# Performance work log

Measured on AMD Instinct MI355X. Metric: run time of the kernel, lower is better.

Reference implementation:

```python
import jax, jax.numpy as jnp
import numpy as np

N, T, K, R, DK = 4096, 8, 4, 8, 64
S = 2   # slot_dim (2D coords)
B = 20  # noise samples (hardcoded in original forward)


def _conv1d(x, w, b, pad):
    # x: [batch, Cin, L], w: [Cout, Cin, ks] (torch Conv1d layout == OIH)
    y = jax.lax.conv_general_dilated(x, w, (1,), [(pad, pad)],
                                     dimension_numbers=('NCH', 'OIH', 'NCH'))
    return y + b[None, :, None]


def setup_inputs() -> dict:
    key = jax.random.key(0)
    ks = iter(jax.random.split(key, 40))
    r = lambda shape, s=0.1: jax.random.normal(next(ks), shape, jnp.float32) * s
    return dict(
        obs=r((1, S, N, T), 1.0),
        obs_vel=r((1, S, N, T), 1.0),
        noise=r((B, 2, 1, 1), 1.0),
        wq_rule=r((S * T, DK)), bq_rule=r((DK,)),
        wq_ctx=r((2 * S * T, DK)), bq_ctx=r((DK,)),
        wk_ctx=r((2 * S * T, DK)), bk_ctx=r((DK,)),
        rule_emb=r((R, DK), 1.0),
        w_noise=r((R,), 1.0), w_indiv=r((R,), 1.0), w_social=r((R,), 1.0),
        sp_w=r((R, S, S * (K + 1), 3)), sp_b=r((R, S)),
        spr_w=r((R, S, S * (K + 1), 1)), spr_b=r((R, S)),
        tp_w=r((R, 12, T, 3)), tp_b=r((R, 12)),
        tpr_w=r((R, 12, T, 1)), tpr_b=r((R, 12)),
        spi_w=r((R, S, S, 3)), spi_b=r((R, S)),
        spir_w=r((R, S, S, 1)), spir_b=r((R, S)),
        tpi_w=r((R, 12, T, 3)), tpi_b=r((R, 12)),
        tpir_w=r((R, 12, T, 1)), tpir_b=r((R, 12)),
    )


def reference(obs, obs_vel, noise, wq_rule, bq_rule, wq_ctx, bq_ctx, wk_ctx, bk_ctx,
              rule_emb, w_noise, w_indiv, w_social,
              sp_w, sp_b, spr_w, spr_b, tp_w, tp_b, tpr_w, tpr_b,
              spi_w, spi_b, spir_w, spir_b, tpi_w, tpi_b, tpir_w, tpir_b):
    # ---- context selection (eval path: topk_onehot) ----
    cat = jnp.concatenate([obs, obs_vel], axis=1)[0]           # [2S, N, T]
    x_ctx = jnp.transpose(cat, (1, 2, 0)).reshape(N, -1)       # [N, T*2S]
    q = x_ctx @ wq_ctx + bq_ctx
    k_ = x_ctx @ wk_ctx + bk_ctx
    attn_ctx = jax.nn.softmax(q @ k_.T, axis=-1)               # [N, N]
    _, ctx_idx = jax.lax.top_k(attn_ctx, K)                    # [N, K]
    # gather == bmm with one-hot [N,N] masks in the original
    ov_node = jnp.transpose(obs_vel[0], (1, 0, 2))             # [N, S, T]
    ctx_vel = ov_node[ctx_idx]                                 # [N, K, S, T]
    ctx_vel = jnp.transpose(ctx_vel, (1, 2, 0, 3)).reshape(1, K * S, N, T)

    # ---- rule selection (hard top-1) ----
    x_rule = jnp.transpose(obs_vel[0], (1, 2, 0)).reshape(N, -1)  # [N, T*S]
    rq = x_rule @ wq_rule + bq_rule
    attn_rule = jax.nn.softmax(rq @ rule_emb.T, axis=-1)       # [N, R]
    rule_mask = jax.nn.one_hot(jnp.argmax(attn_rule, -1), R, dtype=obs.dtype)  # [N, R]

    noise_rep = jnp.tile(noise, (1, K, 1, 1))                  # [B, K*S, 1, 1]

    def rule_fn(wn, wi, ws, p):
        ov = obs_vel + noise * wn                              # [B, S, N, T]
        ov_f = jnp.transpose(ov, (0, 2, 1, 3)).reshape(B * N, S, T)
        cv = ctx_vel + noise_rep * wn                          # [B, K*S, N, T]
        cv_f = jnp.transpose(cv, (0, 2, 1, 3)).reshape(B * N, K * S, T)
        comb = jnp.concatenate([ov_f, cv_f], axis=1)           # [B*N, S*(K+1), T]
        si = jax.nn.relu(_conv1d(ov_f, p['spi_w'], p['spi_b'], 1)) \
             + _conv1d(ov_f, p['spir_w'], p['spir_b'], 0)      # [B*N, S, T]
        ti = jnp.transpose(si, (0, 2, 1))                      # [B*N, T, S]
        indiv = _conv1d(ti, p['tpi_w'], p['tpi_b'], 1) + _conv1d(ti, p['tpir_w'], p['tpir_b'], 0)
        ss = jax.nn.relu(_conv1d(comb, p['sp_w'], p['sp_b'], 1)) \
             + _conv1d(comb, p['spr_w'], p['spr_b'], 0)        # [B*N, S, T]
        ts = jnp.transpose(ss, (0, 2, 1))
        social = _conv1d(ts, p['tp_w'], p['tp_b'], 1) + _conv1d(ts, p['tpr_w'], p['tpr_b'], 0)
        return wi * indiv + ws * social                        # [B*N, 12, S]

    params = dict(sp_w=sp_w, sp_b=sp_b, spr_w=spr_w, spr_b=spr_b,
                  tp_w=tp_w, tp_b=tp_b, tpr_w=tpr_w, tpr_b=tpr_b,
                  spi_w=spi_w, spi_b=spi_b, spir_w=spir_w, spir_b=spir_b,
                  tpi_w=tpi_w, tpi_b=tpi_b, tpir_w=tpir_w, tpir_b=tpir_b)
    preds = jax.vmap(rule_fn)(w_noise, w_indiv, w_social, params)  # [R, B*N, 12, S]
    preds = preds.reshape(R, B, N, 12, S)
    # hard rule dispatch + final permute(0,2,3,1) of the original -> [B, N, 12, S]
    return jnp.einsum('rbnts,nr->bnts', preds, rule_mask)
```

## Files before the change

### kernel.cpp

```cpp
#include <hip/hip_runtime.h>
#include <cstdint>
#include <cstddef>

#define N_   4096
#define T_   8
#define K_   4
#define R_   8
#define DK_  64
#define S_   2
#define B_   20
#define NT_  (N_*T_)

__device__ __forceinline__ unsigned long long mkkey(float v, int col) {
    unsigned u = __float_as_uint(v);
    u = (u & 0x80000000u) ? ~u : (u | 0x80000000u);
    return ((unsigned long long)u << 32) | (unsigned)(~col);
}

#define INS4(t0,t1,t2,t3,keyexpr) do {                                  \
    unsigned long long _k = (keyexpr);                                  \
    if (_k > (t3)) {                                                    \
        bool _g2 = _k > (t2), _g1 = _k > (t1), _g0 = _k > (t0);         \
        (t3) = _g2 ? (t2) : _k;                                         \
        (t2) = _g2 ? (_g1 ? (t1) : _k) : (t2);                          \
        (t1) = _g1 ? (_g0 ? (t0) : _k) : (t1);                          \
        (t0) = _g0 ? _k : (t0);                                         \
    }                                                                   \
} while (0)

__global__ __launch_bounds__(64) void proj_kernel(
    const float* __restrict__ obs, const float* __restrict__ obsv,
    const float* __restrict__ wq_ctx, const float* __restrict__ bq_ctx,
    const float* __restrict__ wk_ctx, const float* __restrict__ bk_ctx,
    const float* __restrict__ wq_rule, const float* __restrict__ bq_rule,
    const float* __restrict__ rule_emb,
    float* __restrict__ qg, float* __restrict__ kg, int* __restrict__ rid)
{
    int n = blockIdx.x;
    int d = threadIdx.x;
    __shared__ float x[32];
    if (d < 32) {
        int t = d >> 2, c = d & 3;
        const float* src = (c < 2) ? obs : obsv;
        x[d] = src[(c & 1) * NT_ + n * T_ + t];
    }
    __syncthreads();
    float q = bq_ctx[d], k = bk_ctx[d], rq = bq_rule[d];
    #pragma unroll
    for (int i = 0; i < 32; ++i) {
        float xv = x[i];
        q = fmaf(xv, wq_ctx[i*64 + d], q);
        k = fmaf(xv, wk_ctx[i*64 + d], k);
    }
    #pragma unroll
    for (int i = 0; i < 16; ++i) {
        int t = i >> 1, s = i & 1;
        rq = fmaf(x[t*4 + 2 + s], wq_rule[i*64 + d], rq);
    }
    qg[n*64 + d] = q;
    kg[n*64 + d] = k;

    float best = -1e30f; int bestr = 0;
    #pragma unroll
    for (int r = 0; r < 8; ++r) {
        float p = rq * rule_emb[r*64 + d];
        #pragma unroll
        for (int off = 32; off > 0; off >>= 1) p += __shfl_xor(p, off, 64);
        if (p > best) { best = p; bestr = r; }
    }
    if (d == 0) rid[n] = bestr;
}

#define BM      16
#define CT      128
#define NSPLIT  4
#define KST     68
#define TILES   ((N_/NSPLIT)/CT)

__global__ __launch_bounds__(256) void attn_topk_kernel(
    const float* __restrict__ qg, const float* __restrict__ kg,
    unsigned long long* __restrict__ part)
{
    __shared__ union U {
        float ks[CT*KST];
        unsigned long long sc[BM*64*4];
    } u;
    __shared__ float qs[BM*64];

    int tid  = threadIdx.x;
    int lane = tid & 63, wv = tid >> 6;
    int rowblk = blockIdx.x / NSPLIT, split = blockIdx.x % NSPLIT;
    int row0 = rowblk * BM;
    int col0 = split * (N_ / NSPLIT);
    int r0 = wv * 4;

    ((float4*)qs)[tid] = ((const float4*)(qg + (size_t)row0*64))[tid];

    unsigned long long T0a=0,T0b=0,T0c=0,T0d=0;
    unsigned long long T1a=0,T1b=0,T1c=0,T1d=0;
    unsigned long long T2a=0,T2b=0,T2c=0,T2d=0;
    unsigned long long T3a=0,T3b=0,T3c=0,T3d=0;

    for (int tile = 0; tile < TILES; ++tile) {
        int c0 = col0 + tile * CT;
        __syncthreads();
        #pragma unroll
        for (int i = 0; i < 8; ++i) {
            int chunk = tid + 256*i;
            int c = chunk >> 4, dseg = chunk & 15;
            float4 v = *(const float4*)(kg + (size_t)(c0 + c)*64 + dseg*4);
            *(float4*)(&u.ks[c*KST + dseg*4]) = v;
        }
        __syncthreads();

        float a00=0.f,a01=0.f, a10=0.f,a11=0.f, a20=0.f,a21=0.f, a30=0.f,a31=0.f;

        #pragma unroll 4
        for (int d = 0; d < 64; d += 4) {
            float4 k0 = *(const float4*)(&u.ks[lane*KST + d]);
            float4 k1 = *(const float4*)(&u.ks[(lane+64)*KST + d]);
            float4 q0 = *(const float4*)(&qs[(r0+0)*64 + d]);
            float4 q1 = *(const float4*)(&qs[(r0+1)*64 + d]);
            float4 q2 = *(const float4*)(&qs[(r0+2)*64 + d]);
            float4 q3 = *(const float4*)(&qs[(r0+3)*64 + d]);
            a00 = fmaf(q0.w,k0.w, fmaf(q0.z,k0.z, fmaf(q0.y,k0.y, fmaf(q0.x,k0.x, a00))));
            a01 = fmaf(q0.w,k1.w, fmaf(q0.z,k1.z, fmaf(q0.y,k1.y, fmaf(q0.x,k1.x, a01))));
            a10 = fmaf(q1.w,k0.w, fmaf(q1.z,k0.z, fmaf(q1.y,k0.y, fmaf(q1.x,k0.x, a10))));
            a11 = fmaf(q1.w,k1.w, fmaf(q1.z,k1.z, fmaf(q1.y,k1.y, fmaf(q1.x,k1.x, a11))));
            a20 = fmaf(q2.w,k0.w, fmaf(q2.z,k0.z, fmaf(q2.y,k0.y, fmaf(q2.x,k0.x, a20))));
            a21 = fmaf(q2.w,k1.w, fmaf(q2.z,k1.z, fmaf(q2.y,k1.y, fmaf(q2.x,k1.x, a21))));
            a30 = fmaf(q3.w,k0.w, fmaf(q3.z,k0.z, fmaf(q3.y,k0.y, fmaf(q3.x,k0.x, a30))));
            a31 = fmaf(q3.w,k1.w, fmaf(q3.z,k1.z, fmaf(q3.y,k1.y, fmaf(q3.x,k1.x, a31))));
        }
        int cA = c0 + lane, cB = c0 + lane + 64;
        INS4(T0a,T0b,T0c,T0d, mkkey(a00, cA));
        INS4(T0a,T0b,T0c,T0d, mkkey(a01, cB));
        INS4(T1a,T1b,T1c,T1d, mkkey(a10, cA));
        INS4(T1a,T1b,T1c,T1d, mkkey(a11, cB));
        INS4(T2a,T2b,T2c,T2d, mkkey(a20, cA));
        INS4(T2a,T2b,T2c,T2d, mkkey(a21, cB));
        INS4(T3a,T3b,T3c,T3d, mkkey(a30, cA));
        INS4(T3a,T3b,T3c,T3d, mkkey(a31, cB));
    }

    __syncthreads();
    {
        unsigned long long* p = &u.sc[((size_t)(r0+0)*64 + lane)*4];
        p[0]=T0a; p[1]=T0b; p[2]=T0c; p[3]=T0d;
        p = &u.sc[((size_t)(r0+1)*64 + lane)*4];
        p[0]=T1a; p[1]=T1b; p[2]=T1c; p[3]=T1d;
        p = &u.sc[((size_t)(r0+2)*64 + lane)*4];
        p[0]=T2a; p[1]=T2b; p[2]=T2c; p[3]=T2d;
        p = &u.sc[((size_t)(r0+3)*64 + lane)*4];
        p[0]=T3a; p[1]=T3b; p[2]=T3c; p[3]=T3d;
    }
    __syncthreads();

    if (tid < BM) {
        unsigned long long m0=0,m1=0,m2=0,m3=0;
        const unsigned long long* p = &u.sc[(size_t)tid*64*4];
        for (int j = 0; j < 256; ++j) INS4(m0,m1,m2,m3, p[j]);
        int n = row0 + tid;
        unsigned long long* q = &part[(size_t)(n*NSPLIT + split)*4];
        q[0]=m0; q[1]=m1; q[2]=m2; q[3]=m3;
    }
}

__global__ __launch_bounds__(256) void merge_kernel(
    const unsigned long long* __restrict__ part, int* __restrict__ cidx)
{
    int n = blockIdx.x * blockDim.x + threadIdx.x;
    if (n >= N_) return;
    unsigned long long m0=0,m1=0,m2=0,m3=0;
    #pragma unroll
    for (int j = 0; j < NSPLIT*4; ++j) INS4(m0,m1,m2,m3, part[(size_t)n*NSPLIT*4 + j]);
    cidx[n*4 + 0] = (int)(~((unsigned)(m0 & 0xffffffffull)));
    cidx[n*4 + 1] = (int)(~((unsigned)(m1 & 0xffffffffull)));
    cidx[n*4 + 2] = (int)(~((unsigned)(m2 & 0xffffffffull)));
    cidx[n*4 + 3] = (int)(~((unsigned)(m3 & 0xffffffffull)));
}

#define WST 708

__global__ __launch_bounds__(256) void predict_kernel(
    const float* __restrict__ obsv, const float* __restrict__ noise,
    const float* __restrict__ w_noise, const float* __restrict__ w_indiv,
    const float* __restrict__ w_social,
    const float* __restrict__ sp_w, const float* __restrict__ sp_b,
    const float* __restrict__ spr_w, const float* __restrict__ spr_b,
    const float* __restrict__ tp_w, const float* __restrict__ tp_b,
    const float* __restrict__ tpr_w, const float* __restrict__ tpr_b,
    const float* __restrict__ spi_w, const float* __restrict__ spi_b,
    const float* __restrict__ spir_w, const float* __restrict__ spir_b,
    const float* __restrict__ tpi_w, const float* __restrict__ tpi_b,
    const float* __restrict__ tpir_w, const float* __restrict__ tpir_b,
    const int* __restrict__ rid, const int* __restrict__ cidx,
    float* __restrict__ out)
{
    __shared__ float W[R_*WST];
    __shared__ float nz_s[B_*2];
    __shared__ float wn_s[R_], wi_s[R_], ws_s[R_];
    int tid = threadIdx.x;

    for (int idx = tid; idx < R_*704; idx += 256) {
        int r = idx / 704, o = idx % 704;
        float v;
        if (o < 12)      v = spi_w[r*12 + o];
        else if (o < 16) v = spir_w[r*4 + (o-12)];
        else if (o < 76) v = sp_w[r*60 + (o-16)];
        else if (o < 96) v = spr_w[r*20 + (o-76)];
        else if (o < 192) { int q=o-96;  int t=q/12, co=q%12; v = tpi_w[((r*12+co)*8+t)*3+1] + tpir_w[(r*12+co)*8+t]; }
        else if (o < 288) { int q=o-192; int t=q/12, co=q%12; v = tpi_w[((r*12+co)*8+t)*3+2]; }
        else if (o < 384) { int q=o-288; int t=q/12, co=q%12; v = tpi_w[((r*12+co)*8+t)*3+0]; }
        else if (o < 480) { int q=o-384; int t=q/12, co=q%12; v = tp_w[((r*12+co)*8+t)*3+1] + tpr_w[(r*12+co)*8+t]; }
        else if (o < 576) { int q=o-480; int t=q/12, co=q%12; v = tp_w[((r*12+co)*8+t)*3+2]; }
        else if (o < 672) { int q=o-576; int t=q/12, co=q%12; v = tp_w[((r*12+co)*8+t)*3+0]; }
        else if (o < 674) v = spi_b[r*2 + (o-672)];
        else if (o < 676) v = spir_b[r*2 + (o-674)];
        else if (o < 678) v = sp_b[r*2 + (o-676)];
        else if (o < 680) v = spr_b[r*2 + (o-678)];
        else if (o < 692) v = tpi_b[r*12 + (o-680)] + tpir_b[r*12 + (o-680)];
        else              v = tp_b[r*12 + (o-692)] + tpr_b[r*12 + (o-692)];
        W[r*WST + o] = v;
    }
    if (tid < B_*2)                  nz_s[tid] = noise[tid];
    if (tid >= 64  && tid < 64+R_)   wn_s[tid-64]  = w_noise[tid-64];
    if (tid >= 96  && tid < 96+R_)   wi_s[tid-96]  = w_indiv[tid-96];
    if (tid >= 128 && tid < 128+R_)  ws_s[tid-128] = w_social[tid-128];
    __syncthreads();

    int item = blockIdx.x*256 + tid;
    if (item >= B_*N_) return;
    int n = item / B_, b = item - n*B_;
    int r = rid[n];
    const float* Wr = &W[r*WST];
    float wn = wn_s[r];
    float nz0 = nz_s[b*2+0]*wn, nz1 = nz_s[b*2+1]*wn;

    float x[10][8];
    #pragma unroll
    for (int s = 0; s < 2; ++s) {
        float4 a = *(const float4*)(obsv + s*NT_ + n*8);
        float4 c = *(const float4*)(obsv + s*NT_ + n*8 + 4);
        float nz = s ? nz1 : nz0;
        x[s][0]=a.x+nz; x[s][1]=a.y+nz; x[s][2]=a.z+nz; x[s][3]=a.w+nz;
        x[s][4]=c.x+nz; x[s][5]=c.y+nz; x[s][6]=c.z+nz; x[s][7]=c.w+nz;
    }
    #pragma unroll
    for (int k = 0; k < 4; ++k) {
        int cn = cidx[n*4 + k];
        #pragma unroll
        for (int s = 0; s < 2; ++s) {
            float4 a = *(const float4*)(obsv + s*NT_ + cn*8);
            float4 c = *(const float4*)(obsv + s*NT_ + cn*8 + 4);
            float nz = s ? nz1 : nz0;
            int ch = 2 + k*2 + s;
            x[ch][0]=a.x+nz; x[ch][1]=a.y+nz; x[ch][2]=a.z+nz; x[ch][3]=a.w+nz;
            x[ch][4]=c.x+nz; x[ch][5]=c.y+nz; x[ch][6]=c.z+nz; x[ch][7]=c.w+nz;
        }
    }

    float si[2][8];
    #pragma unroll
    for (int so = 0; so < 2; ++so) {
        float pre[8];
        float bb = Wr[672+so];
        #pragma unroll
        for (int t = 0; t < 8; ++t) pre[t] = bb;
        #pragma unroll
        for (int ci = 0; ci < 2; ++ci) {
            float w0 = Wr[so*6+ci*3+0], w1 = Wr[so*6+ci*3+1], w2 = Wr[so*6+ci*3+2];
            pre[0] += x[ci][0]*w1 + x[ci][1]*w2;
            #pragma unroll
            for (int t = 1; t < 7; ++t) pre[t] += x[ci][t-1]*w0 + x[ci][t]*w1 + x[ci][t+1]*w2;
            pre[7] += x[ci][6]*w0 + x[ci][7]*w1;
        }
        float l0 = Wr[12+so*2+0], l1 = Wr[12+so*2+1];
        float lb = Wr[674+so];
        #pragma unroll
        for (int t = 0; t < 8; ++t)
            si[so][t] = fmaxf(pre[t], 0.f) + lb + x[0][t]*l0 + x[1][t]*l1;
    }

    float ss[2][8];
    #pragma unroll
    for (int so = 0; so < 2; ++so) {
        float pre[8], lin[8];
        float bb = Wr[676+so], lb = Wr[678+so];
        #pragma unroll
        for (int t = 0; t < 8; ++t) { pre[t] = bb; lin[t] = lb; }
        #pragma unroll
        for (int ci = 0; ci < 10; ++ci) {
            float w0 = Wr[16+so*30+ci*3+0], w1 = Wr[16+so*30+ci*3+1], w2 = Wr[16+so*30+ci*3+2];
            float lw = Wr[76+so*10+ci];
            pre[0] += x[ci][0]*w1 + x[ci][1]*w2;
            #pragma unroll
            for (int t = 1; t < 7; ++t) pre[t] += x[ci][t-1]*w0 + x[ci][t]*w1 + x[ci][t+1]*w2;
            pre[7] += x[ci][6]*w0 + x[ci][7]*w1;
            #pragma unroll
            for (int t = 0; t < 8; ++t) lin[t] += x[ci][t]*lw;
        }
        #pragma unroll
        for (int t = 0; t < 8; ++t) ss[so][t] = fmaxf(pre[t], 0.f) + lin[t];
    }

    float i0[12], i1[12], s0a[12], s1a[12];
    #pragma unroll
    for (int co = 0; co < 12; ++co) {
        float bi = Wr[680+co], bs = Wr[692+co];
        i0[co]=bi; i1[co]=bi; s0a[co]=bs; s1a[co]=bs;
    }
    #pragma unroll
    for (int t = 0; t < 8; ++t) {
        float a0 = si[0][t], a1 = si[1][t];
        float b0 = ss[0][t], b1 = ss[1][t];
        #pragma unroll
        for (int co = 0; co < 12; ++co) {
            i0[co]  += a0*Wr[96 +t*12+co] + a1*Wr[192+t*12+co];
            i1[co]  += a1*Wr[96 +t*12+co] + a0*Wr[288+t*12+co];
            s0a[co] += b0*Wr[384+t*12+co] + b1*Wr[480+t*12+co];
            s1a[co] += b1*Wr[384+t*12+co] + b0*Wr[576+t*12+co];
        }
    }

    float wi = wi_s[r], wsoc = ws_s[r];
    float o[24];
    #pragma unroll
    for (int co = 0; co < 12; ++co) {
        o[co*2+0] = wi*i0[co] + wsoc*s0a[co];
        o[co*2+1] = wi*i1[co] + wsoc*s1a[co];
    }
    float* dst = out + (size_t)(b*N_ + n)*24;
    #pragma unroll
    for (int q4 = 0; q4 < 6; ++q4)
        *(float4*)(dst + q4*4) = *(const float4*)(&o[q4*4]);
}

extern "C" void kernel_launch(void* const* d_in, const int* in_sizes, int n_in,
                              void* d_out, int out_size, void* d_ws, size_t ws_size,
                              hipStream_t stream)
{
    const float* obs      = (const float*)d_in[0];
    const float* obsv     = (const float*)d_in[1];
    const float* noise    = (const float*)d_in[2];
    const float* wq_rule  = (const float*)d_in[3];
    const float* bq_rule  = (const float*)d_in[4];
    const float* wq_ctx   = (const float*)d_in[5];
    const float* bq_ctx   = (const float*)d_in[6];
    const float* wk_ctx   = (const float*)d_in[7];
    const float* bk_ctx   = (const float*)d_in[8];
    const float* rule_emb = (const float*)d_in[9];
    const float* w_noise  = (const float*)d_in[10];
    const float* w_indiv  = (const float*)d_in[11];
    const float* w_social = (const float*)d_in[12];
    const float* sp_w  = (const float*)d_in[13];
    const float* sp_b  = (const float*)d_in[14];
    const float* spr_w = (const float*)d_in[15];
    const float* spr_b = (const float*)d_in[16];
    const float* tp_w  = (const float*)d_in[17];
    const float* tp_b  = (const float*)d_in[18];
    const float* tpr_w = (const float*)d_in[19];
    const float* tpr_b = (const float*)d_in[20];
    const float* spi_w  = (const float*)d_in[21];
    const float* spi_b  = (const float*)d_in[22];
    const float* spir_w = (const float*)d_in[23];
    const float* spir_b = (const float*)d_in[24];
    const float* tpi_w  = (const float*)d_in[25];
    const float* tpi_b  = (const float*)d_in[26];
    const float* tpir_w = (const float*)d_in[27];
    const float* tpir_b = (const float*)d_in[28];

    char* ws = (char*)d_ws;
    float* qg = (float*)(ws);
    float* kg = (float*)(ws + 1048576);
    unsigned long long* part = (unsigned long long*)(ws + 2097152);
    int* rid  = (int*)(ws + 2621440);
    int* cidx = (int*)(ws + 2637824);

    hipLaunchKernelGGL(proj_kernel, dim3(N_), dim3(64), 0, stream,
        obs, obsv, wq_ctx, bq_ctx, wk_ctx, bk_ctx, wq_rule, bq_rule, rule_emb,
        qg, kg, rid);

    hipLaunchKernelGGL(attn_topk_kernel, dim3((N_/BM)*NSPLIT), dim3(256), 0, stream,
        qg, kg, part);

    hipLaunchKernelGGL(merge_kernel, dim3(N_/256), dim3(256), 0, stream,
        part, cidx);

    hipLaunchKernelGGL(predict_kernel, dim3((B_*N_)/256), dim3(256), 0, stream,
        obsv, noise, w_noise, w_indiv, w_social,
        sp_w, sp_b, spr_w, spr_b, tp_w, tp_b, tpr_w, tpr_b,
        spi_w, spi_b, spir_w, spir_b, tpi_w, tpi_b, tpir_w, tpir_b,
        rid, cidx, (float*)d_out);
}
```

Before: 238.5 us.

## Use 4x4 register-blocked outer-product tiling for attention top-k scoring

Rewrites the QK^T score kernel from per-wave 4-row dot products over a 16-row block into a 64x64 tile where each thread computes a 4x4 outer-product block. Q and K are stored transposed in shared memory so each d step needs only two float4 loads for 16 FMAs. The column space is split 16 ways instead of 4, which changes the grid, enlarges the partial-top-k buffer and moves workspace offsets. This cuts shared-memory traffic per FMA, at the cost of strided scalar transposed stores into LDS and a longer merge over 64 partial candidates per row.

```diff
diff --git a/kernel.cpp b/kernel.cpp
--- a/kernel.cpp
+++ b/kernel.cpp
@@ -71,97 +71,114 @@
     if (d == 0) rid[n] = bestr;
 }
 
-#define BM      16
-#define CT      128
-#define NSPLIT  4
-#define KST     68
-#define TILES   ((N_/NSPLIT)/CT)
+#define RPB     64
+#define CTILE   64
+#define NSPLIT  16
+#define DPAD    68
+#define SCP     65
 
 __global__ __launch_bounds__(256) void attn_topk_kernel(
     const float* __restrict__ qg, const float* __restrict__ kg,
     unsigned long long* __restrict__ part)
 {
+    __shared__ float qT[DK_*DPAD];
     __shared__ union U {
-        float ks[CT*KST];
-        unsigned long long sc[BM*64*4];
+        float kT[DK_*DPAD];
+        unsigned long long sc[RPB*SCP];
     } u;
-    __shared__ float qs[BM*64];
-
-    int tid  = threadIdx.x;
-    int lane = tid & 63, wv = tid >> 6;
-    int rowblk = blockIdx.x / NSPLIT, split = blockIdx.x % NSPLIT;
-    int row0 = rowblk * BM;
-    int col0 = split * (N_ / NSPLIT);
-    int r0 = wv * 4;
-
-    ((float4*)qs)[tid] = ((const float4*)(qg + (size_t)row0*64))[tid];
+
+    int tid = threadIdx.x;
+    int tx = tid & 15, ty = tid >> 4;
+    int rowblk = blockIdx.x >> 4, split = blockIdx.x & 15;
+    int row0 = rowblk * RPB;
+    int colbase = split * (N_ / NSPLIT);
+
+    #pragma unroll
+    for (int i = 0; i < 4; ++i) {
+        int chunk = tid + 256*i;
+        int row = chunk & 63, dchunk = chunk >> 6;
+        float4 v = *(const float4*)(qg + (size_t)(row0 + row)*64 + 4*dchunk);
+        u.kT[0] = u.kT[0];
+        qT[(4*dchunk+0)*DPAD + row] = v.x;
+        qT[(4*dchunk+1)*DPAD + row] = v.y;
+        qT[(4*dchunk+2)*DPAD + row] = v.z;
+        qT[(4*dchunk+3)*DPAD + row] = v.w;
+    }
 
     unsigned long long T0a=0,T0b=0,T0c=0,T0d=0;
     unsigned long long T1a=0,T1b=0,T1c=0,T1d=0;
     unsigned long long T2a=0,T2b=0,T2c=0,T2d=0;
     unsigned long long T3a=0,T3b=0,T3c=0,T3d=0;
 
-    for (int tile = 0; tile < TILES; ++tile) {
-        int c0 = col0 + tile * CT;
+    for (int tile = 0; tile < (N_/NSPLIT)/CTILE; ++tile) {
+        int c0 = colbase + tile * CTILE;
         __syncthreads();
         #pragma unroll
-        for (int i = 0; i < 8; ++i) {
+        for (int i = 0; i < 4; ++i) {
             int chunk = tid + 256*i;
-            int c = chunk >> 4, dseg = chunk & 15;
-            float4 v = *(const float4*)(kg + (size_t)(c0 + c)*64 + dseg*4);
-            *(float4*)(&u.ks[c*KST + dseg*4]) = v;
+            int col = chunk & 63, dchunk = chunk >> 6;
+            float4 v = *(const float4*)(kg + (size_t)(c0 + col)*64 + 4*dchunk);
+            u.kT[(4*dchunk+0)*DPAD + col] = v.x;
+            u.kT[(4*dchunk+1)*DPAD + col] = v.y;
+            u.kT[(4*dchunk+2)*DPAD + col] = v.z;
+            u.kT[(4*dchunk+3)*DPAD + col] = v.w;
         }
         __syncthreads();
 
-        float a00=0.f,a01=0.f, a10=0.f,a11=0.f, a20=0.f,a21=0.f, a30=0.f,a31=0.f;
+        float c00=0,c01=0,c02=0,c03=0, c10=0,c11=0,c12=0,c13=0;
+        float c20=0,c21=0,c22=0,c23=0, c30=0,c31=0,c32=0,c33=0;
 
         #pragma unroll 4
-        for (int d = 0; d < 64; d += 4) {
-            float4 k0 = *(const float4*)(&u.ks[lane*KST + d]);
-            float4 k1 = *(const float4*)(&u.ks[(lane+64)*KST + d]);
-            float4 q0 = *(const float4*)(&qs[(r0+0)*64 + d]);
-            float4 q1 = *(const float4*)(&qs[(r0+1)*64 + d]);
-            float4 q2 = *(const float4*)(&qs[(r0+2)*64 + d]);
-            float4 q3 = *(const float4*)(&qs[(r0+3)*64 + d]);
-            a00 = fmaf(q0.w,k0.w, fmaf(q0.z,k0.z, fmaf(q0.y,k0.y, fmaf(q0.x,k0.x, a00))));
-            a01 = fmaf(q0.w,k1.w, fmaf(q0.z,k1.z, fmaf(q0.y,k1.y, fmaf(q0.x,k1.x, a01))));
-            a10 = fmaf(q1.w,k0.w, fmaf(q1.z,k0.z, fmaf(q1.y,k0.y, fmaf(q1.x,k0.x, a10))));
-            a11 = fmaf(q1.w,k1.w, fmaf(q1.z,k1.z, fmaf(q1.y,k1.y, fmaf(q1.x,k1.x, a11))));
-            a20 = fmaf(q2.w,k0.w, fmaf(q2.z,k0.z, fmaf(q2.y,k0.y, fmaf(q2.x,k0.x, a20))));
-            a21 = fmaf(q2.w,k1.w, fmaf(q2.z,k1.z, fmaf(q2.y,k1.y, fmaf(q2.x,k1.x, a21))));
-            a30 = fmaf(q3.w,k0.w, fmaf(q3.z,k0.z, fmaf(q3.y,k0.y, fmaf(q3.x,k0.x, a30))));
-            a31 = fmaf(q3.w,k1.w, fmaf(q3.z,k1.z, fmaf(q3.y,k1.y, fmaf(q3.x,k1.x, a31))));
-        }
-        int cA = c0 + lane, cB = c0 + lane + 64;
-        INS4(T0a,T0b,T0c,T0d, mkkey(a00, cA));
-        INS4(T0a,T0b,T0c,T0d, mkkey(a01, cB));
-        INS4(T1a,T1b,T1c,T1d, mkkey(a10, cA));
-        INS4(T1a,T1b,T1c,T1d, mkkey(a11, cB));
-        INS4(T2a,T2b,T2c,T2d, mkkey(a20, cA));
-        INS4(T2a,T2b,T2c,T2d, mkkey(a21, cB));
-        INS4(T3a,T3b,T3c,T3d, mkkey(a30, cA));
-        INS4(T3a,T3b,T3c,T3d, mkkey(a31, cB));
+        for (int d = 0; d < 64; ++d) {
+            float4 a = *(const float4*)(&qT[d*DPAD + 4*ty]);
+            float4 b = *(const float4*)(&u.kT[d*DPAD + 4*tx]);
+            c00 = fmaf(a.x, b.x, c00); c01 = fmaf(a.x, b.y, c01);
+            c02 = fmaf(a.x, b.z, c02); c03 = fmaf(a.x, b.w, c03);
+            c10 = fmaf(a.y, b.x, c10); c11 = fmaf(a.y, b.y, c11);
+            c12 = fmaf(a.y, b.z, c12); c13 = fmaf(a.y, b.w, c13);
+            c20 = fmaf(a.z, b.x, c20); c21 = fmaf(a.z, b.y, c21);
+            c22 = fmaf(a.z, b.z, c22); c23 = fmaf(a.z, b.w, c23);
+            c30 = fmaf(a.w, b.x, c30); c31 = fmaf(a.w, b.y, c31);
+            c32 = fmaf(a.w, b.z, c32); c33 = fmaf(a.w, b.w, c33);
+        }
+        int cc = c0 + 4*tx;
+        INS4(T0a,T0b,T0c,T0d, mkkey(c00, cc+0));
+        INS4(T0a,T0b,T0c,T0d, mkkey(c01, cc+1));
+        INS4(T0a,T0b,T0c,T0d, mkkey(c02, cc+2));
+        INS4(T0a,T0b,T0c,T0d, mkkey(c03, cc+3));
+        INS4(T1a,T1b,T1c,T1d, mkkey(c10, cc+0));
+        INS4(T1a,T1b,T1c,T1d, mkkey(c11, cc+1));
+        INS4(T1a,T1b,T1c,T1d, mkkey(c12, cc+2));
+        INS4(T1a,T1b,T1c,T1d, mkkey(c13, cc+3));
+        INS4(T2a,T2b,T2c,T2d, mkkey(c20, cc+0));
+        INS4(T2a,T2b,T2c,T2d, mkkey(c21, cc+1));
+        INS4(T2a,T2b,T2c,T2d, mkkey(c22, cc+2));
+        INS4(T2a,T2b,T2c,T2d, mkkey(c23, cc+3));
+        INS4(T3a,T3b,T3c,T3d, mkkey(c30, cc+0));
+        INS4(T3a,T3b,T3c,T3d, mkkey(c31, cc+1));
+        INS4(T3a,T3b,T3c,T3d, mkkey(c32, cc+2));
+        INS4(T3a,T3b,T3c,T3d, mkkey(c33, cc+3));
     }
 
     __syncthreads();
     {
-        unsigned long long* p = &u.sc[((size_t)(r0+0)*64 + lane)*4];
+        unsigned long long* p = &u.sc[(size_t)(4*ty+0)*SCP + 4*tx];
         p[0]=T0a; p[1]=T0b; p[2]=T0c; p[3]=T0d;
-        p = &u.sc[((size_t)(r0+1)*64 + lane)*4];
+        p = &u.sc[(size_t)(4*ty+1)*SCP + 4*tx];
         p[0]=T1a; p[1]=T1b; p[2]=T1c; p[3]=T1d;
-        p = &u.sc[((size_t)(r0+2)*64 + lane)*4];
+        p = &u.sc[(size_t)(4*ty+2)*SCP + 4*tx];
         p[0]=T2a; p[1]=T2b; p[2]=T2c; p[3]=T2d;
-        p = &u.sc[((size_t)(r0+3)*64 + lane)*4];
+        p = &u.sc[(size_t)(4*ty+3)*SCP + 4*tx];
         p[0]=T3a; p[1]=T3b; p[2]=T3c; p[3]=T3d;
     }
     __syncthreads();
 
-    if (tid < BM) {
+    if (tid < RPB) {
         unsigned long long m0=0,m1=0,m2=0,m3=0;
-        const unsigned long long* p = &u.sc[(size_t)tid*64*4];
-        for (int j = 0; j < 256; ++j) INS4(m0,m1,m2,m3, p[j]);
-        int n = row0 + tid;
-        unsigned long long* q = &part[(size_t)(n*NSPLIT + split)*4];
+        const unsigned long long* p = &u.sc[(size_t)tid*SCP];
+        #pragma unroll 8
+        for (int j = 0; j < 64; ++j) INS4(m0,m1,m2,m3, p[j]);
+        unsigned long long* q = &part[(size_t)((row0 + tid)*NSPLIT + split)*4];
         q[0]=m0; q[1]=m1; q[2]=m2; q[3]=m3;
     }
 }
@@ -172,7 +189,7 @@
     int n = blockIdx.x * blockDim.x + threadIdx.x;
     if (n >= N_) return;
     unsigned long long m0=0,m1=0,m2=0,m3=0;
-    #pragma unroll
+    #pragma unroll 8
     for (int j = 0; j < NSPLIT*4; ++j) INS4(m0,m1,m2,m3, part[(size_t)n*NSPLIT*4 + j]);
     cidx[n*4 + 0] = (int)(~((unsigned)(m0 & 0xffffffffull)));
     cidx[n*4 + 1] = (int)(~((unsigned)(m1 & 0xffffffffull)));
@@ -374,14 +391,14 @@
     float* qg = (float*)(ws);
     float* kg = (float*)(ws + 1048576);
     unsigned long long* part = (unsigned long long*)(ws + 2097152);
-    int* rid  = (int*)(ws + 2621440);
-    int* cidx = (int*)(ws + 2637824);
+    int* rid  = (int*)(ws + 4194304);
+    int* cidx = (int*)(ws + 4210688);
 
     hipLaunchKernelGGL(proj_kernel, dim3(N_), dim3(64), 0, stream,
         obs, obsv, wq_ctx, bq_ctx, wk_ctx, bk_ctx, wq_rule, bq_rule, rule_emb,
         qg, kg, rid);
 
-    hipLaunchKernelGGL(attn_topk_kernel, dim3((N_/BM)*NSPLIT), dim3(256), 0, stream,
+    hipLaunchKernelGGL(attn_topk_kernel, dim3((N_/RPB)*NSPLIT), dim3(256), 0, stream,
         qg, kg, part);
 
     hipLaunchKernelGGL(merge_kernel, dim3(N_/256), dim3(256), 0, stream,
```

After: 226.7 us. -4.9%, faster.
